# Optimization experiments

Measured on AMD Instinct MI355X. Metric: run time of the kernel, lower is better.

Reference implementation:

```python
import jax, jax.numpy as jnp
import numpy as np

EPS = 1e-5
K_NN = 10


def _lin_params(key, fan_in, fan_out):
    bound = 1.0 / np.sqrt(fan_in)
    kw, kb = jax.random.split(key)
    w = jax.random.uniform(kw, (fan_in, fan_out), minval=-bound, maxval=bound, dtype=jnp.float32)
    b = jax.random.uniform(kb, (fan_out,), minval=-bound, maxval=bound, dtype=jnp.float32)
    return w, b


def setup_inputs() -> dict:
    key = jax.random.key(0)
    ks = jax.random.split(key, 16)
    C, E = 2, 32  # config_size, embed_size
    P, NF, NC = 512, 50000, 50000
    N = P + NF + NC  # 100512
    NE = 300000

    inp = {}
    inp["path"] = jax.random.normal(ks[0], (P, C), dtype=jnp.float32)
    inp["free"] = jax.random.normal(ks[1], (NF, C), dtype=jnp.float32)
    inp["collided"] = jax.random.normal(ks[2], (NC, C), dtype=jnp.float32)
    inp["obstacles"] = jax.random.normal(ks[3], (10, 6), dtype=jnp.float32)
    inp["edge_index"] = jax.random.randint(ks[4], (2, NE), 0, N, dtype=jnp.int32)
    inp["loop"] = 5

    # node_code: Lin(C+3, E) -> BN(E) -> ReLU -> Lin(E, E)
    inp["nc_w1"], inp["nc_b1"] = _lin_params(ks[5], C + 3, E)
    inp["nc_gamma"] = jnp.ones((E,), jnp.float32)
    inp["nc_beta"] = jnp.zeros((E,), jnp.float32)
    inp["nc_w2"], inp["nc_b2"] = _lin_params(ks[6], E, E)
    # MPNN lin_0: Lin(3E, E) -> ReLU -> Lin(E, E)
    inp["mp0_w1"], inp["mp0_b1"] = _lin_params(ks[7], 3 * E, E)
    inp["mp0_w2"], inp["mp0_b2"] = _lin_params(ks[8], E, E)
    # MPNN lin_1: Lin(E, E) -> ReLU -> Lin(E, E)
    inp["mp1_w1"], inp["mp1_b1"] = _lin_params(ks[9], E, E)
    inp["mp1_w2"], inp["mp1_b2"] = _lin_params(ks[10], E, E)
    # smooth_node: Lin(E, C)
    inp["sn_w"], inp["sn_b"] = _lin_params(ks[11], E, C)
    return inp


def _forward(path, free, collided, obstacles, edge_index, loop,
             nc_w1, nc_b1, nc_gamma, nc_beta, nc_w2, nc_b2,
             mp0_w1, mp0_b1, mp0_w2, mp0_b2,
             mp1_w1, mp1_b1, mp1_w2, mp1_b2,
             sn_w, sn_b):
    scale = 1.0
    path = path / scale
    free = free / scale
    collided = collided / scale

    P = path.shape[0]
    NF = free.shape[0]
    cand = jnp.concatenate([free, collided], axis=0)  # nodes[len(path):], fixed
    M = cand.shape[0]
    N = P + M

    # info one-hot flags (fixed across loops)
    info = jnp.zeros((N, 3), jnp.float32)
    info = info.at[:P, 0].set(1.0)
    info = info.at[P:P + NF, 1].set(1.0)
    info = info.at[P + NF:, 2].set(1.0)

    src0 = edge_index[0].astype(jnp.int32)
    dst0 = edge_index[1].astype(jnp.int32)

    cand_sq = jnp.sum(cand * cand, axis=-1)  # [M]

    def node_code(x):
        h = x @ nc_w1 + nc_b1
        mean = jnp.mean(h, axis=0)
        var = jnp.mean((h - mean) ** 2, axis=0)  # biased, as torch BN training
        h = (h - mean) * jax.lax.rsqrt(var + EPS) * nc_gamma + nc_beta
        h = jax.nn.relu(h)
        return h @ nc_w2 + nc_b2

    for _ in range(loop):
        # kNN: 10 nearest candidates for each path node (non-differentiable)
        p = jax.lax.stop_gradient(path)
        d2 = (jnp.sum(p * p, axis=-1)[:, None] + cand_sq[None, :]
              - 2.0 * p @ jax.lax.stop_gradient(cand).T)  # [P, M]
        _, idx = jax.lax.top_k(-d2, K_NN)  # [P, K]
        src_new = (idx + P).reshape(-1).astype(jnp.int32)
        dst_new = jnp.repeat(jnp.arange(P, dtype=jnp.int32), K_NN)
        src = jnp.concatenate([src0, src_new])
        dst = jnp.concatenate([dst0, dst_new])

        # coalesce: keep only first occurrence of each (src, dst) pair
        order = jnp.lexsort((dst, src))
        ss, ds = src[order], dst[order]
        first = jnp.concatenate([jnp.array([True]),
                                 (ss[1:] != ss[:-1]) | (ds[1:] != ds[:-1])])
        keep = jnp.zeros(src.shape[0], bool).at[order].set(first)

        nodes = jnp.concatenate([path, cand], axis=0)  # [N, C]
        x = node_code(jnp.concatenate([nodes, info], axis=-1))  # [N, E]

        # MPNN message: cat([x_j - x_i, x_j, x_i]) -> lin_0, scatter-add to i
        x_i = x[dst]
        x_j = x[src]
        z = jnp.concatenate([x_j - x_i, x_j, x_i], axis=-1)  # [Etot, 3E]
        m = jax.nn.relu(z @ mp0_w1 + mp0_b1) @ mp0_w2 + mp0_b2
        m = m * keep[:, None].astype(m.dtype)  # zero duplicate edges
        out = jax.ops.segment_sum(m, dst, num_segments=N)
        h = x + (jax.nn.relu(out @ mp1_w1 + mp1_b1) @ mp1_w2 + mp1_b2)

        sm = h[:P] @ sn_w + sn_b  # [P, C]
        path = path.at[1:-1].set(sm[1:-1])

    return path * scale


def reference(path, free, collided, obstacles, edge_index, loop,
              nc_w1, nc_b1, nc_gamma, nc_beta, nc_w2, nc_b2,
              mp0_w1, mp0_b1, mp0_w2, mp0_b2,
              mp1_w1, mp1_b1, mp1_w2, mp1_b2,
              sn_w, sn_b):
    return _forward(path, free, collided, obstacles, edge_index, loop,
                    nc_w1, nc_b1, nc_gamma, nc_beta, nc_w2, nc_b2,
                    mp0_w1, mp0_b1, mp0_w2, mp0_b2,
                    mp1_w1, mp1_b1, mp1_w2, mp1_b2,
                    sn_w, sn_b)
```

## Files before the change

kernel.cpp:

```cpp
#include <hip/hip_runtime.h>
#include <stdint.h>

#define PN     512
#define NFREE  50000
#define NCND   100000
#define NNODE  100512
#define NEDGE  300000
#define KK     10
#define NLOOP  5
#define EPSV   1e-5f

#define GRID   128
#define NCELL  (GRID*GRID)

#define XMINF  (-6.f)
#define YMINF  (-6.f)
#define SPANF  12.f
#define IVCW   ((float)GRID / SPANF)

#define HSIZE  8192
#define HMASK  (HSIZE-1)
#define E0CAP  4096
#define EMPTYK 0xFFFFFFFFFFFFFFFFull

#define NCB    ((NCND+255)/256)
#define NEB    ((NEDGE+255)/256)

#define OFF_HASH    ((size_t)0)
#define OFF_CPOS    (OFF_HASH    + (size_t)HSIZE*8)
#define OFF_SCND    (OFF_CPOS    + 800000)
#define OFF_CSTART  (OFF_SCND    + 1600000)
#define OFF_COFS    (OFF_CSTART  + 65600)
#define OFF_MOM     (OFF_COFS    + 65600)
#define OFF_WCU     (OFF_MOM     + 64)
#define OFF_WCV     (OFF_WCU     + 4096)
#define OFF_BU      (OFF_WCV     + 4096)
#define OFF_BV      (OFF_BU      + 128)
#define OFF_CPATH   (OFF_BV      + 128)
#define OFF_CFREE   (OFF_CPATH   + 128)
#define OFF_CCOL    (OFF_CFREE   + 128)
#define OFF_PATH    (OFF_CCOL    + 128)
#define OFF_E0S     (OFF_PATH    + 4096)
#define OFF_E0D     (OFF_E0S     + (size_t)E0CAP*4)
#define OFF_DEG0    (OFF_E0D     + (size_t)E0CAP*4)
#define OFF_E0C     (OFF_DEG0    + 2048)
#define OFF_E0START (OFF_E0C     + 64)
#define OFF_E0OFS   (OFF_E0START + 2112)
#define OFF_E0CSRS  (OFF_E0OFS   + 2048)

#define OFF_PATH2   OFF_E0S

#define WS_F(o)  ((float*)(ws + (o)))
#define WS_I(o)  ((int*)(ws + (o)))
#define WS_H(o)  ((unsigned long long*)(ws + (o)))

__device__ __forceinline__ bool lexless(float da, int ia, float db, int ib) {
  return (da < db) || (da == db && ia < ib);
}

__device__ __forceinline__ uint32_t hslot(unsigned long long key) {
  return (uint32_t)((key * 0x9E3779B97F4A7C15ull) >> 40) & HMASK;
}

__device__ __forceinline__ void bn_from_moments(const char* ws,
    float w0, float w1, float cp, float clsF, float clsC,
    float pm0, float pm1, float pm00, float pm11, float pm01,
    float* meano, float* rstdo) {
  const float* M = (const float*)(ws + OFF_MOM);
  float sF0=M[0], sF1=M[1], sF00=M[2], sF11=M[3], sF01=M[4];
  float sC0=M[5], sC1=M[6], sC00=M[7], sC11=M[8], sC01=M[9];
  const float NC = (float)(NCND - NFREE);
  float sh  = w0*(sF0+sC0+pm0) + w1*(sF1+sC1+pm1)
            + (float)NFREE*clsF + NC*clsC + (float)PN*cp;
  float sh2 = w0*w0*(sF00+sC00+pm00) + w1*w1*(sF11+sC11+pm11)
            + 2.f*w0*w1*(sF01+sC01+pm01)
            + 2.f*w0*(clsF*sF0 + clsC*sC0 + cp*pm0)
            + 2.f*w1*(clsF*sF1 + clsC*sC1 + cp*pm1)
            + (float)NFREE*clsF*clsF + NC*clsC*clsC + (float)PN*cp*cp;
  float mean = sh  * (1.f / NNODE);
  float ex2  = sh2 * (1.f / NNODE);
  float var  = ex2 - mean * mean;
  *meano = mean;
  *rstdo = 1.0f / sqrtf(var + EPSV);
}

#define INSERT10(d2v, jv)                                                  \
  if (lexless((d2v), (jv), bd[9], bi[9])) {                                \
    bool placed = false;                                                   \
    _Pragma("unroll")                                                      \
    for (int k = 9; k > 0; k--) {                                          \
      bool shift = !placed && lexless((d2v), (jv), bd[k-1], bi[k-1]);      \
      bool here  = !placed && !shift;                                      \
      if (here)       { bd[k] = (d2v); bi[k] = (jv); placed = true; }      \
      else if (shift) { bd[k] = bd[k-1]; bi[k] = bi[k-1]; }                \
    }                                                                      \
    if (!placed) { bd[0] = (d2v); bi[0] = (jv); }                          \
  }

#define WSTORE10(base) do {                                                \
    float cd[10]; int ci[10];                                              \
    _Pragma("unroll")                                                      \
    for (int k = 0; k < 10; k++) { cd[k] = bd[k]; ci[k] = bi[k]; }         \
    _Pragma("unroll")                                                      \
    for (int r = 0; r < 10; r++) {                                         \
      float md = cd[0]; int mi = ci[0];                                    \
      _Pragma("unroll")                                                    \
      for (int off = 32; off >= 1; off >>= 1) {                            \
        float od = __shfl_xor(md, off);                                    \
        int   oi = __shfl_xor(mi, off);                                    \
        if (lexless(od, oi, md, mi)) { md = od; mi = oi; }                 \
      }                                                                    \
      bool win = (cd[0] == md) && (ci[0] == mi);                           \
      if (win) {                                                           \
        _Pragma("unroll")                                                  \
        for (int k = 0; k < 9; k++) { cd[k] = cd[k+1]; ci[k] = ci[k+1]; }  \
        cd[9] = 3.4e38f; ci[9] = 0x7FFFFFFF;                               \
      }                                                                    \
      if (lane == r) { sD[(base)+r] = md; sI[(base)+r] = mi; }             \
    }                                                                      \
  } while (0)

#define MERGE40() do {                                                     \
    float de = (lane < 40) ? sD[lane] : 3.4e38f;                           \
    int   ie = (lane < 40) ? sI[lane] : 0x7FFFFFFF;                        \
    int rank = 0;                                                          \
    for (int f = 0; f < 40; f++) {                                         \
      float df = sD[f]; int iff = sI[f];                                   \
      bool less = lexless(df, iff, de, ie) ||                              \
                  (df == de && iff == ie && f < lane);                     \
      rank += less ? 1 : 0;                                                \
    }                                                                      \
    if (lane < 40 && rank < 10) { sMD[rank] = de; sMI[rank] = ie; }        \
  } while (0)

#define SCAN_BOX4(xA, xB, yA, yB) do {                                     \
    for (int _y = (yA) + wv; _y <= (yB); _y += 4) {                        \
      int _s = cst[_y*GRID + (xA)], _e = cst[_y*GRID + (xB) + 1];          \
      for (int _t = _s + lane; _t < _e; _t += 64) {                        \
        float4 _q = scnd[_t];                                              \
        float _d2 = (psq + _q.z) - 2.f * fmaf(p1, _q.y, p0 * _q.x);        \
        int _j = __float_as_int(_q.w);                                     \
        INSERT10(_d2, _j);                                                 \
      }                                                                    \
    }                                                                      \
  } while (0)


__global__ __launch_bounds__(256) void k_init0(char* __restrict__ ws,
                                               const float* __restrict__ path_in) {
  unsigned i = blockIdx.x * 256u + threadIdx.x;
  if (i < HSIZE)   WS_H(OFF_HASH)[i] = EMPTYK;
  if (i < NCELL+1) WS_I(OFF_CSTART)[i] = 0;
  if (i < 1024)    WS_F(OFF_PATH)[i] = path_in[i];
  if (i < 512)     WS_I(OFF_DEG0)[i] = 0;
  if (i < 16)      WS_F(OFF_MOM)[i] = 0.f;
  if (i == 0)      *WS_I(OFF_E0C) = 0;
}

__global__ __launch_bounds__(256) void k_setupA(char* __restrict__ ws,
    const float* __restrict__ freep, const float* __restrict__ collp,
    const int* __restrict__ ei,
    const float* __restrict__ ncw1, const float* __restrict__ ncb1,
    const float* __restrict__ m0w1, const float* __restrict__ m0b1,
    const float* __restrict__ ncw2, const float* __restrict__ ncb2) {
  int b = blockIdx.x, tid = threadIdx.x;
  if (b < NCB) {
    __shared__ float s10[4][10];
    int j = b*256 + tid;
    bool valid = (j < NCND);
    float c0 = 0.f, c1 = 0.f;
    if (valid) {
      if (j < NFREE) { c0 = freep[2*j];          c1 = freep[2*j+1]; }
      else           { c0 = collp[2*(j-NFREE)];  c1 = collp[2*(j-NFREE)+1]; }
      ((float2*)(ws + OFF_CPOS))[j] = make_float2(c0, c1);
    }
    bool isF = valid && (j < NFREE), isC = valid && (j >= NFREE);
    float v[10];
    v[0]=isF?c0:0.f; v[1]=isF?c1:0.f; v[2]=isF?c0*c0:0.f; v[3]=isF?c1*c1:0.f; v[4]=isF?c0*c1:0.f;
    v[5]=isC?c0:0.f; v[6]=isC?c1:0.f; v[7]=isC?c0*c0:0.f; v[8]=isC?c1*c1:0.f; v[9]=isC?c0*c1:0.f;
    #pragma unroll
    for (int q = 0; q < 10; q++)
      #pragma unroll
      for (int off = 32; off >= 1; off >>= 1) v[q] += __shfl_xor(v[q], off);
    int wv = tid >> 6, lane = tid & 63;
    if (lane == 0) {
      #pragma unroll
      for (int q = 0; q < 10; q++) s10[wv][q] = v[q];
    }
    if (valid) {
      int cx = min(GRID-1, max(0, (int)((c0 - XMINF) * IVCW)));
      int cy = min(GRID-1, max(0, (int)((c1 - YMINF) * IVCW)));
      atomicAdd(&WS_I(OFF_CSTART)[cy*GRID + cx], 1);
    }
    __syncthreads();
    if (tid < 10)
      atomicAdd(&WS_F(OFF_MOM)[tid], s10[0][tid]+s10[1][tid]+s10[2][tid]+s10[3][tid]);
  } else if (b < NCB + NEB) {
    int e = (b - NCB)*256 + tid;
    if (e >= NEDGE) return;
    int src = ei[e], dst = ei[NEDGE + e];
    if (dst >= PN) return;
    unsigned long long key = (unsigned long long)src * NNODE + (unsigned long long)dst;
    unsigned long long* hash = WS_H(OFF_HASH);
    uint32_t slot = hslot(key);
    for (;;) {
      unsigned long long prev = atomicCAS(&hash[slot], EMPTYK, key);
      if (prev == EMPTYK) {
        int pos = atomicAdd(WS_I(OFF_E0C), 1);
        if (pos < E0CAP) {
          WS_I(OFF_E0S)[pos] = src;
          WS_I(OFF_E0D)[pos] = dst;
          atomicAdd(&WS_I(OFF_DEG0)[dst], 1);
        }
        break;
      }
      if (prev == key) break;
      slot = (slot + 1) & HMASK;
    }
  } else {
    __shared__ float Wu[1024], Wv[1024];
    for (int it = 0; it < 4; it++) {
      int idx = it*256 + tid, k = idx >> 5, g = idx & 31;
      float a = m0w1[k*32+g], b2 = m0w1[(k+32)*32+g], c = m0w1[(k+64)*32+g];
      Wu[idx] = a + b2;  Wv[idx] = c - a;
    }
    __syncthreads();
    for (int it = 0; it < 4; it++) {
      int idx = it*256 + tid, k = idx >> 5, g = idx & 31;
      float au = 0.f, av = 0.f;
      #pragma unroll
      for (int f = 0; f < 32; f++) {
        float w2 = ncw2[k*32+f];
        au = fmaf(w2, Wu[f*32+g], au);
        av = fmaf(w2, Wv[f*32+g], av);
      }
      WS_F(OFF_WCU)[idx] = au;  WS_F(OFF_WCV)[idx] = av;
    }
    if (tid < 32) {
      float bu = 0.f, bv = 0.f;
      #pragma unroll
      for (int f = 0; f < 32; f++) {
        bu = fmaf(ncb2[f], Wu[f*32+tid], bu);
        bv = fmaf(ncb2[f], Wv[f*32+tid], bv);
      }
      WS_F(OFF_BU)[tid] = bu;
      WS_F(OFF_BV)[tid] = bv + m0b1[tid];
      WS_F(OFF_CPATH)[tid] = ncw1[64+tid]  + ncb1[tid];
      WS_F(OFF_CFREE)[tid] = ncw1[96+tid]  + ncb1[tid];
      WS_F(OFF_CCOL)[tid]  = ncw1[128+tid] + ncb1[tid];
    }
  }
}

__global__ __launch_bounds__(256) void k_scan2(char* __restrict__ ws) {
  int b = blockIdx.x, tid = threadIdx.x;
  if (b == 0) {
    __shared__ int part[256];
    int* cnt = WS_I(OFF_CSTART);
    int base = tid * (NCELL/256);
    int sum = 0;
    for (int k = 0; k < NCELL/256; k++) sum += cnt[base+k];
    part[tid] = sum;
    __syncthreads();
    for (int off = 1; off < 256; off <<= 1) {
      int t = (tid >= off) ? part[tid - off] : 0;
      __syncthreads();
      part[tid] += t;
      __syncthreads();
    }
    int run = part[tid] - sum;
    for (int k = 0; k < NCELL/256; k++) {
      int c = cnt[base+k];
      cnt[base+k] = run;
      WS_I(OFF_COFS)[base+k] = run;
      run += c;
    }
    if (tid == 255) cnt[NCELL] = run;
  } else {
    __shared__ int sc[512];
    sc[tid]     = WS_I(OFF_DEG0)[tid];
    sc[256+tid] = WS_I(OFF_DEG0)[256+tid];
    __syncthreads();
    if (tid == 0) {
      int run = 0;
      for (int i = 0; i < 512; i++) { int c = sc[i]; sc[i] = run; run += c; }
      WS_I(OFF_E0START)[512] = run;
    }
    __syncthreads();
    WS_I(OFF_E0START)[tid]     = sc[tid];
    WS_I(OFF_E0START)[256+tid] = sc[256+tid];
    WS_I(OFF_E0OFS)[tid]       = sc[tid];
    WS_I(OFF_E0OFS)[256+tid]   = sc[256+tid];
    __syncthreads();
    int n = *WS_I(OFF_E0C); if (n > E0CAP) n = E0CAP;
    for (int e = tid; e < n; e += 256) {
      int dst = WS_I(OFF_E0D)[e];
      int pos = atomicAdd(&WS_I(OFF_E0OFS)[dst], 1);
      WS_I(OFF_E0CSRS)[pos] = WS_I(OFF_E0S)[e];
    }
  }
}

__global__ __launch_bounds__(256) void k_scatter(char* __restrict__ ws) {
  int j = blockIdx.x * 256 + threadIdx.x;
  if (j >= NCND) return;
  float2 c = ((const float2*)(ws + OFF_CPOS))[j];
  int cx = min(GRID-1, max(0, (int)((c.x - XMINF) * IVCW)));
  int cy = min(GRID-1, max(0, (int)((c.y - YMINF) * IVCW)));
  int pos = atomicAdd(&WS_I(OFF_COFS)[cy*GRID + cx], 1);
  ((float4*)(ws + OFF_SCND))[pos] =
      make_float4(c.x, c.y, c.x*c.x + c.y*c.y, __int_as_float(j));
}

__global__ __launch_bounds__(256, 2) void k_loop_v2(char* __restrict__ ws,
    const float* __restrict__ ncw1, const float* __restrict__ gamma,
    const float* __restrict__ beta, const float* __restrict__ ncw2,
    const float* __restrict__ ncb2, const float* __restrict__ m0w2,
    const float* __restrict__ m0b2, const float* __restrict__ m1w1,
    const float* __restrict__ m1b1, const float* __restrict__ m1w2,
    const float* __restrict__ m1b2, const float* __restrict__ snw,
    const float* __restrict__ snb, float* __restrict__ outp, int l) {
  __shared__ float sD[40];
  __shared__ int   sI[40];
  __shared__ float sMD[10];
  __shared__ int   sMI[10];
  __shared__ int   sbox[9];
  __shared__ int   sRC[4];
  __shared__ float sS[4][32];
  int tid = threadIdx.x, lane = tid & 63, wv = tid >> 6;
  int node = blockIdx.x;
  const float4* scnd = (const float4*)(ws + OFF_SCND);
  const int* cst = WS_I(OFF_CSTART);

  int fA = lane & 31;
  const float w0 = ncw1[fA], w1 = ncw1[32+fA];
  const float cp   = WS_F(OFF_CPATH)[fA];
  const float clsF = WS_F(OFF_CFREE)[fA];
  const float clsC = WS_F(OFF_CCOL)[fA];
  const float gm = gamma[fA], bt = beta[fA];
  const float buf = WS_F(OFF_BU)[fA];
  const float bvf = WS_F(OFF_BV)[fA];
  const float* wcu = WS_F(OFF_WCU);
  const float* wcv = WS_F(OFF_WCV);
  const int s0 = WS_I(OFF_E0START)[node], s1 = WS_I(OFF_E0START)[node+1];
  const int nfix = s1 - s0;
  const int fsrc = (lane < nfix) ? WS_I(OFF_E0CSRS)[s0 + lane] : -1;

  float* pcur = WS_F((l & 1) ? OFF_PATH2 : OFF_PATH);
  float* pnxt = WS_F((l & 1) ? OFF_PATH  : OFF_PATH2);
  float p0 = pcur[2*node], p1 = pcur[2*node+1];
  float psq = p0*p0 + p1*p1;

  int cx = min(GRID-1, max(0, (int)((p0 - XMINF) * IVCW)));
  int cy = min(GRID-1, max(0, (int)((p1 - YMINF) * IVCW)));
  {
    int Rw = 1 << wv;
    int xA = max(cx-Rw, 0), xB = min(cx+Rw, GRID-1);
    int yA = max(cy-Rw, 0), yB = min(cy+Rw, GRID-1);
    int cnt = 0;
    for (int y = yA + lane; y <= yB; y += 64)
      cnt += cst[y*GRID + xB + 1] - cst[y*GRID + xA];
    #pragma unroll
    for (int off = 32; off >= 1; off >>= 1) cnt += __shfl_xor(cnt, off);
    if (lane == 0) sRC[wv] = cnt;
  }
  __syncthreads();
  if (wv == 0) {
    int R = 0;
    if (sRC[3] >= KK) R = 8;
    if (sRC[2] >= KK) R = 4;
    if (sRC[1] >= KK) R = 2;
    if (sRC[0] >= KK) R = 1;
    int xLa, xRa, yLa, yRa;
    if (R == 0) {
      R = 16;
      for (;;) {
        xLa = max(cx-R, 0); xRa = min(cx+R, GRID-1);
        yLa = max(cy-R, 0); yRa = min(cy+R, GRID-1);
        int cnt = 0;
        for (int y = yLa + lane; y <= yRa; y += 64)
          cnt += cst[y*GRID + xRa + 1] - cst[y*GRID + xLa];
        #pragma unroll
        for (int off = 32; off >= 1; off >>= 1) cnt += __shfl_xor(cnt, off);
        if (cnt >= KK || R >= GRID) break;
        R <<= 1;
      }
    } else {
      xLa = max(cx-R, 0); xRa = min(cx+R, GRID-1);
      yLa = max(cy-R, 0); yRa = min(cy+R, GRID-1);
    }
    if (lane == 0) { sbox[0]=xLa; sbox[1]=xRa; sbox[2]=yLa; sbox[3]=yRa; }
  }
  __syncthreads();
  int xL = sbox[0], xR = sbox[1], yL = sbox[2], yR = sbox[3];

  float bd[10]; int bi[10];
  #pragma unroll
  for (int k = 0; k < 10; k++) { bd[k] = 3.4e38f; bi[k] = 0x7FFFFFFF; }
  SCAN_BOX4(xL, xR, yL, yR);
  WSTORE10(wv*10);
  __syncthreads();
  if (wv == 0) MERGE40();
  __syncthreads();

  if (tid == 0) {
    float r = sqrtf(sMD[9]) * 1.000002f;
    int xL2 = min(GRID-1, max(0, (int)((p0 - r - XMINF) * IVCW)));
    int xR2 = min(GRID-1, max(0, (int)((p0 + r - XMINF) * IVCW)));
    int yL2 = min(GRID-1, max(0, (int)((p1 - r - YMINF) * IVCW)));
    int yR2 = min(GRID-1, max(0, (int)((p1 + r - YMINF) * IVCW)));
    sbox[4]=xL2; sbox[5]=xR2; sbox[6]=yL2; sbox[7]=yR2;
    sbox[8] = (xL2 >= xL && xR2 <= xR && yL2 >= yL && yR2 <= yR) ? 1 : 0;
  }
  __syncthreads();
  if (!sbox[8]) {
    int xL2 = sbox[4], xR2 = sbox[5], yL2 = sbox[6], yR2 = sbox[7];
    #pragma unroll
    for (int k = 0; k < 10; k++) { bd[k] = 3.4e38f; bi[k] = 0x7FFFFFFF; }
    SCAN_BOX4(xL2, xR2, yL2, yR2);
    WSTORE10(wv*10);
    __syncthreads();
    if (wv == 0) MERGE40();
    __syncthreads();
  }


  int selIdx = (lane < KK) ? sMI[lane] : 0;
  int srcg   = (lane < KK) ? selIdx + PN : -1;
  int keep   = (lane < KK) ? 1 : 0;
  for (int t = 0; t < min(nfix, 64); t++) {
    int fs = __shfl(fsrc, t);
    if (fs == srcg) keep = 0;
  }
  for (int t = 64; t < nfix; t++) {
    int fs = WS_I(OFF_E0CSRS)[s0 + t];
    if (fs == srcg) keep = 0;
  }
  unsigned long long kmask = __ballot(keep);
  int deg = (int)__popcll(kmask) + nfix;

  int t2 = lane - KK;
  int srcb = __shfl(fsrc, (t2 & 63));
  float eq0 = 0.f, eq1 = 0.f; int ecl = 1, eva = 0;
  if (lane < KK) {
    eva = keep;
    if (keep) {
      eq0 = WS_F(OFF_CPOS)[2*selIdx];
      eq1 = WS_F(OFF_CPOS)[2*selIdx+1];
      ecl = (selIdx < NFREE) ? 1 : 2;
    }
  } else if (t2 < nfix) {
    eva = 1;
    if (srcb < PN) { eq0 = pcur[2*srcb]; eq1 = pcur[2*srcb+1]; ecl = 0; }
    else {
      int jj = srcb - PN;
      eq0 = WS_F(OFF_CPOS)[2*jj]; eq1 = WS_F(OFF_CPOS)[2*jj+1];
      ecl = (jj < NFREE) ? 1 : 2;
    }
  }

  float pm0=0,pm1=0,pm00=0,pm11=0,pm01=0;
  const float2* pc2 = (const float2*)pcur;
  for (int r2 = lane; r2 < PN; r2 += 64) {
    float2 q = pc2[r2];
    pm0+=q.x; pm1+=q.y; pm00+=q.x*q.x; pm11+=q.y*q.y; pm01+=q.x*q.y;
  }
  #pragma unroll
  for (int off = 32; off >= 1; off >>= 1) {
    pm0+=__shfl_xor(pm0,off); pm1+=__shfl_xor(pm1,off); pm00+=__shfl_xor(pm00,off);
    pm11+=__shfl_xor(pm11,off); pm01+=__shfl_xor(pm01,off);
  }
  float mean, rstd;
  bn_from_moments(ws, w0, w1, cp, clsF, clsC, pm0, pm1, pm00, pm11, pm01,
                  &mean, &rstd);

  float hD = fmaf(p1, w1, fmaf(p0, w0, cp));
  float xnd = fmaf((hD - mean) * rstd, gm, bt);
  xnd = xnd > 0.f ? xnd : 0.f;
  float av = bvf;
  #pragma unroll
  for (int m = 0; m < 32; m++) av = fmaf(__shfl(xnd, m), wcv[m*32+fA], av);

  int hf = lane >> 5;
  int Etot = KK + min(nfix, 54);
  int nT = (Etot + 7) >> 3;
  float S = 0.f;
  for (int t = 0; t < nT; t++) {
    int e  = (t << 3) + (wv << 1) + hf;
    int ee = e & 63;
    int   ev = __shfl(eva, ee);
    float q0 = __shfl(eq0, ee), q1 = __shfl(eq1, ee);
    int   ec = __shfl(ecl, ee);
    float clsv = (ec == 0) ? cp : ((ec == 1) ? clsF : clsC);
    float hq = fmaf(q1, w1, fmaf(q0, w0, clsv));
    float xnf = fmaf((hq - mean) * rstd, gm, bt);
    xnf = xnf > 0.f ? xnf : 0.f;
    float au = buf;
    #pragma unroll
    for (int m = 0; m < 32; m++)
      au = fmaf(__shfl(xnf, m, 32), wcu[m*32+fA], au);
    float rr = au + av;
    if (e < Etot && ev && rr > 0.f) S += rr;
  }
  S += __shfl_xor(S, 32);
  if (lane < 32) sS[wv][lane] = S;
  __syncthreads();

  if (wv != 0) return;

  float St = sS[0][fA] + sS[1][fA] + sS[2][fA] + sS[3][fA];
  for (int t = 54; t < nfix; t++) {
    int src = WS_I(OFF_E0CSRS)[s0 + t];
    float q0, q1, clsv;
    if (src < PN) { q0 = pcur[2*src]; q1 = pcur[2*src+1]; clsv = cp; }
    else {
      int jj = src - PN;
      q0 = WS_F(OFF_CPOS)[2*jj]; q1 = WS_F(OFF_CPOS)[2*jj+1];
      clsv = (jj < NFREE) ? clsF : clsC;
    }
    float hq = fmaf(q1, w1, fmaf(q0, w0, clsv));
    float xnf = fmaf((hq - mean) * rstd, gm, bt);
    xnf = xnf > 0.f ? xnf : 0.f;
    float au = buf;
    #pragma unroll
    for (int m = 0; m < 32; m++) au = fmaf(__shfl(xnf, m), wcu[m*32+fA], au);
    float rr = au + av;
    if (rr > 0.f) St += rr;
  }

  float o = (float)deg * m0b2[fA];
  #pragma unroll
  for (int k = 0; k < 32; k++) o = fmaf(__shfl(St, k), m0w2[k*32+fA], o);
  float t1 = m1b1[fA];
  #pragma unroll
  for (int k = 0; k < 32; k++) t1 = fmaf(__shfl(o, k), m1w1[k*32+fA], t1);
  t1 = t1 > 0.f ? t1 : 0.f;
  float g2 = m1b2[fA];
  #pragma unroll
  for (int k = 0; k < 32; k++) g2 = fmaf(__shfl(t1, k), m1w2[k*32+fA], g2);
  float x = ncb2[fA];
  #pragma unroll
  for (int k = 0; k < 32; k++) x = fmaf(__shfl(xnd, k), ncw2[k*32+fA], x);
  float hh = x + g2;
  float r0 = hh * snw[2*fA], r1 = hh * snw[2*fA+1];
  #pragma unroll
  for (int off = 16; off >= 1; off >>= 1) {
    r0 += __shfl_xor(r0, off);
    r1 += __shfl_xor(r1, off);
  }
  if (lane == 0) {
    float np0, np1;
    if (node == 0 || node == PN-1) { np0 = p0; np1 = p1; }
    else { np0 = snb[0] + r0; np1 = snb[1] + r1; }
    if (l == NLOOP-1) { outp[2*node] = np0; outp[2*node+1] = np1; }
    else              { pnxt[2*node] = np0; pnxt[2*node+1] = np1; }
  }
}


extern "C" void kernel_launch(void* const* d_in, const int* in_sizes, int n_in,
                              void* d_out, int out_size, void* d_ws, size_t ws_size,
                              hipStream_t stream) {
  const float* path  = (const float*)d_in[0];
  const float* freep = (const float*)d_in[1];
  const float* collp = (const float*)d_in[2];
  const int*   ei    = (const int*)d_in[4];
  const float* ncw1  = (const float*)d_in[6];
  const float* ncb1  = (const float*)d_in[7];
  const float* gamma = (const float*)d_in[8];
  const float* beta  = (const float*)d_in[9];
  const float* ncw2  = (const float*)d_in[10];
  const float* ncb2  = (const float*)d_in[11];
  const float* m0w1  = (const float*)d_in[12];
  const float* m0b1  = (const float*)d_in[13];
  const float* m0w2  = (const float*)d_in[14];
  const float* m0b2  = (const float*)d_in[15];
  const float* m1w1  = (const float*)d_in[16];
  const float* m1b1  = (const float*)d_in[17];
  const float* m1w2  = (const float*)d_in[18];
  const float* m1b2  = (const float*)d_in[19];
  const float* snw   = (const float*)d_in[20];
  const float* snb   = (const float*)d_in[21];
  char* ws = (char*)d_ws;

  k_init0  <<<65, 256, 0, stream>>>(ws, path);
  k_setupA <<<NCB + NEB + 1, 256, 0, stream>>>(ws, freep, collp, ei,
                                               ncw1, ncb1, m0w1, m0b1, ncw2, ncb2);
  k_scan2  <<<2, 256, 0, stream>>>(ws);
  k_scatter<<<NCB, 256, 0, stream>>>(ws);

  for (int l = 0; l < NLOOP; l++) {
    k_loop_v2<<<PN, 256, 0, stream>>>(ws, ncw1, gamma, beta, ncw2, ncb2,
                                      m0w2, m0b2, m1w1, m1b1, m1w2, m1b2,
                                      snw, snb, (float*)d_out, l);
  }
}
```

Measured before the change: 261.6 us.

## Predict kNN search radius from Gaussian density and drop count pass

Replaces the per-node counting pass, which sized the grid search box by summing cell counts, with an analytic radius estimate. The estimate assumes the candidate points follow a standard 2-D normal density with 100000 points. A doubling fallback loop handles boxes that return fewer than 10 neighbours, and the containment rescan is kept, so results stay exact. The top-10 merge now runs redundantly in every wave, which removes a shared-memory box broadcast and several block barriers. The cost is that the radius heuristic is tuned to the input distribution and can oversize or undersize the box, with extra rescans, on other data.

```diff
diff --git a/kernel.cpp b/kernel.cpp
--- a/kernel.cpp
+++ b/kernel.cpp
@@ -17,6 +17,7 @@
 #define YMINF  (-6.f)
 #define SPANF  12.f
 #define IVCW   ((float)GRID / SPANF)
+#define CW     (SPANF / (float)GRID)
 
 #define HSIZE  8192
 #define HMASK  (HSIZE-1)
@@ -120,7 +121,7 @@
     }                                                                      \
   } while (0)
 
-#define MERGE40() do {                                                     \
+#define MERGE40ALL() do {                                                  \
     float de = (lane < 40) ? sD[lane] : 3.4e38f;                           \
     int   ie = (lane < 40) ? sI[lane] : 0x7FFFFFFF;                        \
     int rank = 0;                                                          \
@@ -143,6 +144,11 @@
         INSERT10(_d2, _j);                                                 \
       }                                                                    \
     }                                                                      \
+  } while (0)
+
+#define BOX_FROM_R(Rv) do {                                                \
+    xL = max(cx-(Rv), 0); xR = min(cx+(Rv), GRID-1);                       \
+    yL = max(cy-(Rv), 0); yR = min(cy+(Rv), GRID-1);                       \
   } while (0)
 
 
@@ -312,7 +318,7 @@
       make_float4(c.x, c.y, c.x*c.x + c.y*c.y, __int_as_float(j));
 }
 
-__global__ __launch_bounds__(256, 2) void k_loop_v2(char* __restrict__ ws,
+__global__ __launch_bounds__(256, 2) void k_loop_v4(char* __restrict__ ws,
     const float* __restrict__ ncw1, const float* __restrict__ gamma,
     const float* __restrict__ beta, const float* __restrict__ ncw2,
     const float* __restrict__ ncb2, const float* __restrict__ m0w2,
@@ -324,8 +330,6 @@
   __shared__ int   sI[40];
   __shared__ float sMD[10];
   __shared__ int   sMI[10];
-  __shared__ int   sbox[9];
-  __shared__ int   sRC[4];
   __shared__ float sS[4][32];
   int tid = threadIdx.x, lane = tid & 63, wv = tid >> 6;
   int node = blockIdx.x;
@@ -348,51 +352,21 @@
 
   float* pcur = WS_F((l & 1) ? OFF_PATH2 : OFF_PATH);
   float* pnxt = WS_F((l & 1) ? OFF_PATH  : OFF_PATH2);
-  float p0 = pcur[2*node], p1 = pcur[2*node+1];
+  float2 pp = *(const float2*)&pcur[2*node];
+  float p0 = pp.x, p1 = pp.y;
   float psq = p0*p0 + p1*p1;
 
   int cx = min(GRID-1, max(0, (int)((p0 - XMINF) * IVCW)));
   int cy = min(GRID-1, max(0, (int)((p1 - YMINF) * IVCW)));
+  int R;
   {
-    int Rw = 1 << wv;
-    int xA = max(cx-Rw, 0), xB = min(cx+Rw, GRID-1);
-    int yA = max(cy-Rw, 0), yB = min(cy+Rw, GRID-1);
-    int cnt = 0;
-    for (int y = yA + lane; y <= yB; y += 64)
-      cnt += cst[y*GRID + xB + 1] - cst[y*GRID + xA];
-    #pragma unroll
-    for (int off = 32; off >= 1; off >>= 1) cnt += __shfl_xor(cnt, off);
-    if (lane == 0) sRC[wv] = cnt;
-  }
-  __syncthreads();
-  if (wv == 0) {
-    int R = 0;
-    if (sRC[3] >= KK) R = 8;
-    if (sRC[2] >= KK) R = 4;
-    if (sRC[1] >= KK) R = 2;
-    if (sRC[0] >= KK) R = 1;
-    int xLa, xRa, yLa, yRa;
-    if (R == 0) {
-      R = 16;
-      for (;;) {
-        xLa = max(cx-R, 0); xRa = min(cx+R, GRID-1);
-        yLa = max(cy-R, 0); yRa = min(cy+R, GRID-1);
-        int cnt = 0;
-        for (int y = yLa + lane; y <= yRa; y += 64)
-          cnt += cst[y*GRID + xRa + 1] - cst[y*GRID + xLa];
-        #pragma unroll
-        for (int off = 32; off >= 1; off >>= 1) cnt += __shfl_xor(cnt, off);
-        if (cnt >= KK || R >= GRID) break;
-        R <<= 1;
-      }
-    } else {
-      xLa = max(cx-R, 0); xRa = min(cx+R, GRID-1);
-      yLa = max(cy-R, 0); yRa = min(cy+R, GRID-1);
-    }
-    if (lane == 0) { sbox[0]=xLa; sbox[1]=xRa; sbox[2]=yLa; sbox[3]=yRa; }
-  }
-  __syncthreads();
-  int xL = sbox[0], xR = sbox[1], yL = sbox[2], yR = sbox[3];
+    float lam = 15915.494f * __expf(-0.5f * psq);
+    float need = __fsqrt_rn(40.f / lam) * (1.f / CW);
+    R = (int)ceilf(0.5f * (need - 1.f));
+    R = min(max(R, 1), 32);
+  }
+  int xL, xR, yL, yR;
+  BOX_FROM_R(R);
 
   float bd[10]; int bi[10];
   #pragma unroll
@@ -400,28 +374,36 @@
   SCAN_BOX4(xL, xR, yL, yR);
   WSTORE10(wv*10);
   __syncthreads();
-  if (wv == 0) MERGE40();
-  __syncthreads();
-
-  if (tid == 0) {
+  MERGE40ALL();
+
+  while (sMD[9] >= 3.3e38f && R < GRID) {
+    R <<= 1;
+    BOX_FROM_R(R);
+    __syncthreads();
+    #pragma unroll
+    for (int k = 0; k < 10; k++) { bd[k] = 3.4e38f; bi[k] = 0x7FFFFFFF; }
+    SCAN_BOX4(xL, xR, yL, yR);
+    WSTORE10(wv*10);
+    __syncthreads();
+    MERGE40ALL();
+  }
+
+  {
     float r = sqrtf(sMD[9]) * 1.000002f;
     int xL2 = min(GRID-1, max(0, (int)((p0 - r - XMINF) * IVCW)));
     int xR2 = min(GRID-1, max(0, (int)((p0 + r - XMINF) * IVCW)));
     int yL2 = min(GRID-1, max(0, (int)((p1 - r - YMINF) * IVCW)));
     int yR2 = min(GRID-1, max(0, (int)((p1 + r - YMINF) * IVCW)));
-    sbox[4]=xL2; sbox[5]=xR2; sbox[6]=yL2; sbox[7]=yR2;
-    sbox[8] = (xL2 >= xL && xR2 <= xR && yL2 >= yL && yR2 <= yR) ? 1 : 0;
-  }
-  __syncthreads();
-  if (!sbox[8]) {
-    int xL2 = sbox[4], xR2 = sbox[5], yL2 = sbox[6], yR2 = sbox[7];
-    #pragma unroll
-    for (int k = 0; k < 10; k++) { bd[k] = 3.4e38f; bi[k] = 0x7FFFFFFF; }
-    SCAN_BOX4(xL2, xR2, yL2, yR2);
-    WSTORE10(wv*10);
-    __syncthreads();
-    if (wv == 0) MERGE40();
-    __syncthreads();
+    bool contained = (xL2 >= xL && xR2 <= xR && yL2 >= yL && yR2 <= yR);
+    if (!contained) {
+      __syncthreads();
+      #pragma unroll
+      for (int k = 0; k < 10; k++) { bd[k] = 3.4e38f; bi[k] = 0x7FFFFFFF; }
+      SCAN_BOX4(xL2, xR2, yL2, yR2);
+      WSTORE10(wv*10);
+      __syncthreads();
+      MERGE40ALL();
+    }
   }
 
 
@@ -590,7 +572,7 @@
   k_scatter<<<NCB, 256, 0, stream>>>(ws);
 
   for (int l = 0; l < NLOOP; l++) {
-    k_loop_v2<<<PN, 256, 0, stream>>>(ws, ncw1, gamma, beta, ncw2, ncb2,
+    k_loop_v4<<<PN, 256, 0, stream>>>(ws, ncw1, gamma, beta, ncw2, ncb2,
                                       m0w2, m0b2, m1w1, m1b1, m1w2, m1b2,
                                       snw, snb, (float*)d_out, l);
   }
```

Measured after the change: 258.7 us. Within noise of the previous version (-1.1%).
